# Optimization experiments

Measured on AMD Instinct MI355X. Metric: run time of the kernel, lower is better.

## Reference

```python
import jax, jax.numpy as jnp
import numpy as np

NUM_EMB = 512
LATENT = 128
TEXT_DIM = 512


def setup_inputs() -> dict:
    key = jax.random.key(0)
    ks = jax.random.split(key, 12)
    B, N = 64, 8192
    x = jax.random.normal(ks[0], (B, N, 3), dtype=jnp.float32)
    s = jax.random.normal(ks[1], (B, N), dtype=jnp.float32)
    e = jax.random.normal(ks[2], (B, TEXT_DIM), dtype=jnp.float32)
    # point_mlp: Linear(4,64) -> ReLU -> Linear(64,128); weights stored (in,out)
    W1 = jax.random.normal(ks[3], (4, 64), dtype=jnp.float32) * 0.5
    b1 = jnp.zeros((64,), dtype=jnp.float32)
    W2 = jax.random.normal(ks[4], (64, 128), dtype=jnp.float32) * 0.125
    b2 = jnp.zeros((128,), dtype=jnp.float32)
    # latent_mlp: Linear(128+512,256) -> ReLU -> Linear(256,128)
    W3 = jax.random.normal(ks[5], (128 + TEXT_DIM, 256), dtype=jnp.float32) * 0.04
    b3 = jnp.zeros((256,), dtype=jnp.float32)
    W4 = jax.random.normal(ks[6], (256, LATENT), dtype=jnp.float32) * 0.0625
    b4 = jnp.zeros((LATENT,), dtype=jnp.float32)
    # codebook init uniform(-1/K, 1/K) as in torch code
    codebook = jax.random.uniform(ks[7], (NUM_EMB, LATENT), dtype=jnp.float32,
                                  minval=-1.0 / NUM_EMB, maxval=1.0 / NUM_EMB)
    return {"x": x, "s": s, "e": e, "W1": W1, "b1": b1, "W2": W2, "b2": b2,
            "W3": W3, "b3": b3, "W4": W4, "b4": b4, "codebook": codebook}


def reference(x, s, e, W1, b1, W2, b2, W3, b3, W4, b4, codebook):
    # PointNet feature extraction
    point_inp = jnp.concatenate([x, s[..., None]], axis=-1)        # (B,N,4)
    h = jax.nn.relu(point_inp @ W1 + b1)                           # (B,N,64)
    point_feat = h @ W2 + b2                                       # (B,N,128)
    global_feat = jnp.max(point_feat, axis=1)                      # (B,128)
    combined = jnp.concatenate([global_feat, e], axis=-1)          # (B,640)
    z_e = jax.nn.relu(combined @ W3 + b3) @ W4 + b4                # (B,latent)
    # VQ: squared-L2 distances to codebook, argmin, gather
    dists = (jnp.sum(z_e * z_e, axis=1, keepdims=True)
             - 2.0 * (z_e @ codebook.T)
             + jnp.sum(codebook * codebook, axis=1))               # (B,K)
    indices = jnp.argmin(dists, axis=1)                            # (B,)
    z_q = codebook[indices]                                        # (B,latent)
    sg = jax.lax.stop_gradient
    codebook_loss = jnp.mean((z_q - sg(z_e)) ** 2)
    commitment_loss = jnp.mean((z_e - sg(z_q)) ** 2)
    z_q_st = z_e + sg(z_q - z_e)
    return (z_q_st, z_e, codebook_loss, commitment_loss, indices)
```

## Files before the change

### kernel.cpp

```cpp
#include <hip/hip_runtime.h>
#include <hip/hip_bf16.h>

typedef unsigned int u32;
typedef __attribute__((ext_vector_type(4))) unsigned int u32x4;
typedef __attribute__((ext_vector_type(8))) short s16x8;
typedef __attribute__((ext_vector_type(4))) float f32x4;

__device__ __forceinline__ u32 rne_hi(float a) {
    u32 u = __float_as_uint(a);
    return (u + 0x7FFFu + ((u >> 16) & 1u)) & 0xFFFF0000u;
}
__device__ __forceinline__ u32 pk_bf16(float a0, float a1) {
    __hip_bfloat162 pk2 = __float22bfloat162_rn(make_float2(a0, a1));
    u32 r;
    __builtin_memcpy(&r, &pk2, 4);
    return r;
}

__global__ __launch_bounds__(256, 4) void k1_pointfeat(
    const float* __restrict__ x, const float* __restrict__ s,
    const float* __restrict__ W1, const float* __restrict__ b1,
    const float* __restrict__ W2, float* __restrict__ ws_part)
{
    __shared__ __align__(16) u32 Hlds[2 * 2 * 64 * 32];
    const int tid   = threadIdx.x;
    const int lane  = tid & 63;
    const int point = tid & 63;
    const int kq    = __builtin_amdgcn_readfirstlane(tid >> 6);
    const int rl    = lane & 15;
    const int kg2   = lane >> 4;

    const int p0 = blockIdx.x * 512;

    s16x8 wbh[2][2], wbl[2][2];
    #pragma unroll
    for (int n = 0; n < 2; ++n)
        #pragma unroll
        for (int sl2 = 0; sl2 < 2; ++sl2)
            #pragma unroll
            for (int j = 0; j < 8; ++j) {
                float f = W2[(size_t)(kg2 * 8 + j + sl2 * 32) * 128 + kq * 32 + n * 16 + rl];
                u32 hb = rne_hi(f);
                float lo = f - __uint_as_float(hb);
                u32 lb = rne_hi(lo);
                wbh[n][sl2][j] = (short)(hb >> 16);
                wbl[n][sl2][j] = (short)(lb >> 16);
            }

    float rmax0 = -3.402823466e38f, rmax1 = -3.402823466e38f;

    const int wr0 = point * 32 + ((2 * kq)     ^ (point & 7)) * 4;
    const int wr1 = point * 32 + ((2 * kq + 1) ^ (point & 7)) * 4;

#define STAGE_COMPUTE(PX, PY, PZ, PW, VH0, VH1, VL0, VL1)                      \
    {                                                                          \
        _Pragma("unroll")                                                      \
        for (int h = 0; h < 2; ++h) {                                          \
            u32 hp[4], lp[4];                                                  \
            _Pragma("unroll")                                                  \
            for (int c = 0; c < 4; ++c) {                                      \
                const int k0 = kq * 16 + h * 8 + c * 2;                        \
                float a0 = fmaf(PX, W1[k0],                                    \
                           fmaf(PY, W1[64 + k0],                               \
                           fmaf(PZ, W1[128 + k0],                              \
                           fmaf(PW, W1[192 + k0], b1[k0]))));                  \
                float a1 = fmaf(PX, W1[k0 + 1],                                \
                           fmaf(PY, W1[65 + k0],                               \
                           fmaf(PZ, W1[129 + k0],                              \
                           fmaf(PW, W1[193 + k0], b1[k0 + 1]))));              \
                a0 = a0 > 0.f ? a0 : 0.f;                                      \
                a1 = a1 > 0.f ? a1 : 0.f;                                      \
                u32 ph = pk_bf16(a0, a1);                                      \
                float h0 = __uint_as_float(ph << 16);                          \
                float h1 = __uint_as_float(ph & 0xFFFF0000u);                  \
                u32 pl = pk_bf16(a0 - h0, a1 - h1);                            \
                hp[c] = ph; lp[c] = pl;                                        \
            }                                                                  \
            if (h == 0) { VH0 = (u32x4){hp[0],hp[1],hp[2],hp[3]};              \
                          VL0 = (u32x4){lp[0],lp[1],lp[2],lp[3]}; }            \
            else        { VH1 = (u32x4){hp[0],hp[1],hp[2],hp[3]};              \
                          VL1 = (u32x4){lp[0],lp[1],lp[2],lp[3]}; }            \
        }                                                                      \
    }
#define STAGE_WRITE(GG, VH0, VH1, VL0, VL1)                                    \
    {                                                                          \
        u32* Hw = &Hlds[((GG) & 1) * 4096];                                    \
        *(u32x4*)(Hw + wr0)        = VH0;                                      \
        *(u32x4*)(Hw + wr1)        = VH1;                                      \
        *(u32x4*)(Hw + 2048 + wr0) = VL0;                                      \
        *(u32x4*)(Hw + 2048 + wr1) = VL1;                                      \
    }

    {
        const int gp = p0 + point;
        float px = x[(size_t)gp * 3 + 0], py = x[(size_t)gp * 3 + 1];
        float pz = x[(size_t)gp * 3 + 2], pw = s[gp];
        u32x4 vh0, vh1, vl0, vl1;
        STAGE_COMPUTE(px, py, pz, pw, vh0, vh1, vl0, vl1)
        STAGE_WRITE(0, vh0, vh1, vl0, vl1)
    }
    float pxn, pyn, pzn, pwn;
    {
        const int gp = p0 + 64 + point;
        pxn = x[(size_t)gp * 3 + 0]; pyn = x[(size_t)gp * 3 + 1];
        pzn = x[(size_t)gp * 3 + 2]; pwn = s[gp];
    }

#define ARD(M, SL2) ((M) * 16 + rl) * 32 + ((((SL2) * 4 + kg2) ^ (rl & 7)) * 4)

    #pragma unroll 1
    for (int g = 0; g < 8; ++g) {
        __syncthreads();
        const u32* Hb = &Hlds[(g & 1) * 4096];

        s16x8 ah0[4], al0[4];
        #pragma unroll
        for (int m = 0; m < 4; ++m) {
            ah0[m] = *(const s16x8*)(Hb + ARD(m, 0));
            al0[m] = *(const s16x8*)(Hb + 2048 + ARD(m, 0));
        }

        u32x4 vh0, vh1, vl0, vl1;
        if (g < 7) {
            STAGE_COMPUTE(pxn, pyn, pzn, pwn, vh0, vh1, vl0, vl1)
        }

        f32x4 acc[4][2] = {};
        #pragma unroll
        for (int m = 0; m < 4; ++m)
            #pragma unroll
            for (int n = 0; n < 2; ++n)
                acc[m][n] = __builtin_amdgcn_mfma_f32_16x16x32_bf16(
                    ah0[m], wbh[n][0], acc[m][n], 0, 0, 0);
        #pragma unroll
        for (int m = 0; m < 4; ++m)
            #pragma unroll
            for (int n = 0; n < 2; ++n)
                acc[m][n] = __builtin_amdgcn_mfma_f32_16x16x32_bf16(
                    ah0[m], wbl[n][0], acc[m][n], 0, 0, 0);
        #pragma unroll
        for (int m = 0; m < 4; ++m)
            #pragma unroll
            for (int n = 0; n < 2; ++n)
                acc[m][n] = __builtin_amdgcn_mfma_f32_16x16x32_bf16(
                    al0[m], wbh[n][0], acc[m][n], 0, 0, 0);

        s16x8 ah1[4], al1[4];
        #pragma unroll
        for (int m = 0; m < 4; ++m) {
            ah1[m] = *(const s16x8*)(Hb + ARD(m, 1));
            al1[m] = *(const s16x8*)(Hb + 2048 + ARD(m, 1));
        }
        if (g < 6) {
            const int gp = p0 + (g + 2) * 64 + point;
            pxn = x[(size_t)gp * 3 + 0]; pyn = x[(size_t)gp * 3 + 1];
            pzn = x[(size_t)gp * 3 + 2]; pwn = s[gp];
        }

        #pragma unroll
        for (int m = 0; m < 4; ++m)
            #pragma unroll
            for (int n = 0; n < 2; ++n)
                acc[m][n] = __builtin_amdgcn_mfma_f32_16x16x32_bf16(
                    ah1[m], wbh[n][1], acc[m][n], 0, 0, 0);
        #pragma unroll
        for (int m = 0; m < 4; ++m)
            #pragma unroll
            for (int n = 0; n < 2; ++n)
                acc[m][n] = __builtin_amdgcn_mfma_f32_16x16x32_bf16(
                    ah1[m], wbl[n][1], acc[m][n], 0, 0, 0);
        #pragma unroll
        for (int m = 0; m < 4; ++m)
            #pragma unroll
            for (int n = 0; n < 2; ++n)
                acc[m][n] = __builtin_amdgcn_mfma_f32_16x16x32_bf16(
                    al1[m], wbh[n][1], acc[m][n], 0, 0, 0);

        if (g < 7) {
            STAGE_WRITE(g + 1, vh0, vh1, vl0, vl1)
        }

        #pragma unroll
        for (int m = 0; m < 4; ++m)
            #pragma unroll
            for (int r = 0; r < 4; ++r) {
                rmax0 = fmaxf(rmax0, acc[m][0][r]);
                rmax1 = fmaxf(rmax1, acc[m][1][r]);
            }
    }
#undef ARD
#undef STAGE_COMPUTE
#undef STAGE_WRITE

    rmax0 = fmaxf(rmax0, __shfl_xor(rmax0, 16, 64));
    rmax0 = fmaxf(rmax0, __shfl_xor(rmax0, 32, 64));
    rmax1 = fmaxf(rmax1, __shfl_xor(rmax1, 16, 64));
    rmax1 = fmaxf(rmax1, __shfl_xor(rmax1, 32, 64));
    if (lane < 16) {
        ws_part[blockIdx.x * 128 + kq * 32 + lane]      = rmax0;
        ws_part[blockIdx.x * 128 + kq * 32 + 16 + lane] = rmax1;
    }
}

__global__ __launch_bounds__(256) void k2a_hidden(
    const float* __restrict__ ws_part, const float* __restrict__ b2,
    const float* __restrict__ e,
    const float* __restrict__ W3, const float* __restrict__ b3,
    float* __restrict__ ws_hid)
{
    const int blk = blockIdx.x;
    const int b   = blk >> 2;
    const int c   = blk & 3;
    const int tid = threadIdx.x;
    const int u   = tid & 63;
    const int part = tid >> 6;
    __shared__ float comb[640];
    __shared__ float psum[4][64];

    for (int i = tid; i < 640; i += 256) {
        float v;
        if (i < 128) {
            const float* __restrict__ pp = ws_part + (size_t)b * 16 * 128 + i;
            float m = pp[0];
            #pragma unroll
            for (int t = 1; t < 16; ++t) m = fmaxf(m, pp[t * 128]);
            v = m + b2[i];
        } else {
            v = e[b * 512 + (i - 128)];
        }
        comb[i] = v;
    }
    __syncthreads();

    const int gu = c * 64 + u;
    const float* __restrict__ Wp = W3 + (size_t)(part * 160) * 256 + gu;
    const float* __restrict__ cp = comb + part * 160;
    float a = 0.f;
    for (int i = 0; i < 160; ++i) a = fmaf(cp[i], Wp[(size_t)i * 256], a);
    psum[part][u] = a;
    __syncthreads();
    if (tid < 64) {
        float hv = psum[0][u] + psum[1][u] + psum[2][u] + psum[3][u] + b3[gu];
        ws_hid[b * 256 + gu] = hv > 0.f ? hv : 0.f;
    }
}

__global__ __launch_bounds__(512) void k2b_vq(
    const float* __restrict__ ws_hid,
    const float* __restrict__ W4, const float* __restrict__ b4,
    const float* __restrict__ cb, float* __restrict__ out,
    float* __restrict__ ws_loss)
{
    const int b = blockIdx.x, tid = threadIdx.x;
    __shared__ float hid[256];
    __shared__ float psum[4][128];
    __shared__ float ze[128];
    __shared__ float red_d[512];
    __shared__ int   red_i[512];
    __shared__ float lred[128];
    __shared__ float zzs;

    if (tid < 256) hid[tid] = ws_hid[b * 256 + tid];
    __syncthreads();

    {
        const int u = tid & 127, part = tid >> 7;
        const float* __restrict__ Wp = W4 + (size_t)(part * 64) * 128 + u;
        const float* __restrict__ hp = hid + part * 64;
        float a = 0.f;
        for (int i = 0; i < 64; ++i) a = fmaf(hp[i], Wp[(size_t)i * 128], a);
        psum[part][u] = a;
    }
    __syncthreads();
    if (tid < 128) {
        float a = psum[0][tid] + psum[1][tid] + psum[2][tid] + psum[3][tid] + b4[tid];
        ze[tid] = a;
        out[8192 + b * 128 + tid] = a;
    }
    __syncthreads();

    if (tid < 64) {
        float t = ze[tid] * ze[tid] + ze[tid + 64] * ze[tid + 64];
        #pragma unroll
        for (int d = 1; d < 64; d <<= 1) t += __shfl_xor(t, d, 64);
        if (tid == 0) zzs = t;
    }
    __syncthreads();

    {
        float dot = 0.f, cc = 0.f;
        const f32x4* __restrict__ cp = (const f32x4*)(cb + (size_t)tid * 128);
        for (int k4 = 0; k4 < 32; ++k4) {
            f32x4 v = cp[k4];
            dot = fmaf(ze[k4 * 4 + 0], v.x, dot);
            cc  = fmaf(v.x, v.x, cc);
            dot = fmaf(ze[k4 * 4 + 1], v.y, dot);
            cc  = fmaf(v.y, v.y, cc);
            dot = fmaf(ze[k4 * 4 + 2], v.z, dot);
            cc  = fmaf(v.z, v.z, cc);
            dot = fmaf(ze[k4 * 4 + 3], v.w, dot);
            cc  = fmaf(v.w, v.w, cc);
        }
        red_d[tid] = zzs - 2.f * dot + cc;
        red_i[tid] = tid;
    }
    __syncthreads();

    for (int sft = 256; sft >= 1; sft >>= 1) {
        if (tid < sft) {
            float da = red_d[tid], db = red_d[tid + sft];
            int   ia = red_i[tid], ib = red_i[tid + sft];
            if (db < da || (db == da && ib < ia)) { red_d[tid] = db; red_i[tid] = ib; }
        }
        __syncthreads();
    }
    const int bc = red_i[0];

    if (tid < 128) {
        float zq  = cb[(size_t)bc * 128 + tid];
        float zev = ze[tid];
        out[b * 128 + tid] = zev + (zq - zev);
        float d = zq - zev;
        lred[tid] = d * d;
    }
    if (tid == 0) out[16386 + b] = (float)bc;
    __syncthreads();
    if (tid < 64) {
        float t = lred[tid] + lred[tid + 64];
        #pragma unroll
        for (int d = 1; d < 64; d <<= 1) t += __shfl_xor(t, d, 64);
        if (tid == 0) ws_loss[b] = t;
    }
}

__global__ void k3_loss(const float* __restrict__ ws_loss, float* __restrict__ out)
{
    const int t = threadIdx.x;
    float v = ws_loss[t];
    #pragma unroll
    for (int d = 1; d < 64; d <<= 1) v += __shfl_xor(v, d, 64);
    if (t == 0) {
        float m = v / 8192.f;
        out[16384] = m;
        out[16385] = m;
    }
}

extern "C" void kernel_launch(void* const* d_in, const int* in_sizes, int n_in,
                              void* d_out, int out_size, void* d_ws, size_t ws_size,
                              hipStream_t stream) {
    const float* x  = (const float*)d_in[0];
    const float* s  = (const float*)d_in[1];
    const float* e  = (const float*)d_in[2];
    const float* W1 = (const float*)d_in[3];
    const float* b1 = (const float*)d_in[4];
    const float* W2 = (const float*)d_in[5];
    const float* b2 = (const float*)d_in[6];
    const float* W3 = (const float*)d_in[7];
    const float* b3 = (const float*)d_in[8];
    const float* W4 = (const float*)d_in[9];
    const float* b4 = (const float*)d_in[10];
    const float* cb = (const float*)d_in[11];
    float* out = (float*)d_out;

    float* ws_part = (float*)d_ws;
    float* ws_hid  = (float*)d_ws + 1024 * 128;
    float* ws_loss = (float*)d_ws + 1024 * 128 + 64 * 256;

    k1_pointfeat<<<1024, 256, 0, stream>>>(x, s, W1, b1, W2, ws_part);
    k2a_hidden<<<256, 256, 0, stream>>>(ws_part, b2, e, W3, b3, ws_hid);
    k2b_vq<<<64, 512, 0, stream>>>(ws_hid, W4, b4, cb, out, ws_loss);
    k3_loss<<<1, 64, 0, stream>>>(ws_loss, out);
}
```

Before: 47.60 us.

## Retile point-MLP MFMA per wave and fuse hidden and VQ head kernels

Each wave in the point-feature kernel now covers a 32-point by 64-channel tile instead of 64 points by 32 channels. That halves the LDS fragment reads per wave but doubles the per-wave W2 register fragments, so occupancy is lowered to 3 blocks per SIMD. Partial maxima are written per M-half, which doubles the partial buffer and the reduction count. The separate latent-MLP hidden kernel and VQ kernel are fused into one 1024-thread block per batch item, removing a launch and the hidden-state round trip through global memory, at the cost of fewer blocks doing the W3 product.

```diff
diff --git a/kernel.cpp b/kernel.cpp
--- a/kernel.cpp
+++ b/kernel.cpp
@@ -17,7 +17,7 @@
     return r;
 }
 
-__global__ __launch_bounds__(256, 4) void k1_pointfeat(
+__global__ __launch_bounds__(256, 3) void k1_pointfeat(
     const float* __restrict__ x, const float* __restrict__ s,
     const float* __restrict__ W1, const float* __restrict__ b1,
     const float* __restrict__ W2, float* __restrict__ ws_part)
@@ -27,19 +27,21 @@
     const int lane  = tid & 63;
     const int point = tid & 63;
     const int kq    = __builtin_amdgcn_readfirstlane(tid >> 6);
+    const int mh    = kq >> 1;
+    const int nh    = kq & 1;
     const int rl    = lane & 15;
     const int kg2   = lane >> 4;
 
     const int p0 = blockIdx.x * 512;
 
-    s16x8 wbh[2][2], wbl[2][2];
+    s16x8 wbh[4][2], wbl[4][2];
     #pragma unroll
-    for (int n = 0; n < 2; ++n)
+    for (int n = 0; n < 4; ++n)
         #pragma unroll
         for (int sl2 = 0; sl2 < 2; ++sl2)
             #pragma unroll
             for (int j = 0; j < 8; ++j) {
-                float f = W2[(size_t)(kg2 * 8 + j + sl2 * 32) * 128 + kq * 32 + n * 16 + rl];
+                float f = W2[(size_t)(kg2 * 8 + j + sl2 * 32) * 128 + nh * 64 + n * 16 + rl];
                 u32 hb = rne_hi(f);
                 float lo = f - __uint_as_float(hb);
                 u32 lb = rne_hi(lo);
@@ -47,7 +49,8 @@
                 wbl[n][sl2][j] = (short)(lb >> 16);
             }
 
-    float rmax0 = -3.402823466e38f, rmax1 = -3.402823466e38f;
+    float rmaxn[4] = {-3.402823466e38f, -3.402823466e38f,
+                      -3.402823466e38f, -3.402823466e38f};
 
     const int wr0 = point * 32 + ((2 * kq)     ^ (point & 7)) * 4;
     const int wr1 = point * 32 + ((2 * kq + 1) ^ (point & 7)) * 4;
@@ -108,16 +111,18 @@
 
 #define ARD(M, SL2) ((M) * 16 + rl) * 32 + ((((SL2) * 4 + kg2) ^ (rl & 7)) * 4)
 
+    const int mh2 = mh * 2;
+
     #pragma unroll 1
     for (int g = 0; g < 8; ++g) {
         __syncthreads();
         const u32* Hb = &Hlds[(g & 1) * 4096];
 
-        s16x8 ah0[4], al0[4];
-        #pragma unroll
-        for (int m = 0; m < 4; ++m) {
-            ah0[m] = *(const s16x8*)(Hb + ARD(m, 0));
-            al0[m] = *(const s16x8*)(Hb + 2048 + ARD(m, 0));
+        s16x8 ah0[2], al0[2];
+        #pragma unroll
+        for (int m = 0; m < 2; ++m) {
+            ah0[m] = *(const s16x8*)(Hb + ARD(mh2 + m, 0));
+            al0[m] = *(const s16x8*)(Hb + 2048 + ARD(mh2 + m, 0));
         }
 
         u32x4 vh0, vh1, vl0, vl1;
@@ -125,31 +130,31 @@
             STAGE_COMPUTE(pxn, pyn, pzn, pwn, vh0, vh1, vl0, vl1)
         }
 
-        f32x4 acc[4][2] = {};
-        #pragma unroll
-        for (int m = 0; m < 4; ++m)
-            #pragma unroll
-            for (int n = 0; n < 2; ++n)
+        f32x4 acc[2][4] = {};
+        #pragma unroll
+        for (int m = 0; m < 2; ++m)
+            #pragma unroll
+            for (int n = 0; n < 4; ++n)
                 acc[m][n] = __builtin_amdgcn_mfma_f32_16x16x32_bf16(
                     ah0[m], wbh[n][0], acc[m][n], 0, 0, 0);
         #pragma unroll
-        for (int m = 0; m < 4; ++m)
-            #pragma unroll
-            for (int n = 0; n < 2; ++n)
+        for (int m = 0; m < 2; ++m)
+            #pragma unroll
+            for (int n = 0; n < 4; ++n)
                 acc[m][n] = __builtin_amdgcn_mfma_f32_16x16x32_bf16(
                     ah0[m], wbl[n][0], acc[m][n], 0, 0, 0);
         #pragma unroll
-        for (int m = 0; m < 4; ++m)
-            #pragma unroll
-            for (int n = 0; n < 2; ++n)
+        for (int m = 0; m < 2; ++m)
+            #pragma unroll
+            for (int n = 0; n < 4; ++n)
                 acc[m][n] = __builtin_amdgcn_mfma_f32_16x16x32_bf16(
                     al0[m], wbh[n][0], acc[m][n], 0, 0, 0);
 
-        s16x8 ah1[4], al1[4];
-        #pragma unroll
-        for (int m = 0; m < 4; ++m) {
-            ah1[m] = *(const s16x8*)(Hb + ARD(m, 1));
-            al1[m] = *(const s16x8*)(Hb + 2048 + ARD(m, 1));
+        s16x8 ah1[2], al1[2];
+        #pragma unroll
+        for (int m = 0; m < 2; ++m) {
+            ah1[m] = *(const s16x8*)(Hb + ARD(mh2 + m, 1));
+            al1[m] = *(const s16x8*)(Hb + 2048 + ARD(mh2 + m, 1));
         }
         if (g < 6) {
             const int gp = p0 + (g + 2) * 64 + point;
@@ -158,21 +163,21 @@
         }
 
         #pragma unroll
-        for (int m = 0; m < 4; ++m)
-            #pragma unroll
-            for (int n = 0; n < 2; ++n)
+        for (int m = 0; m < 2; ++m)
+            #pragma unroll
+            for (int n = 0; n < 4; ++n)
                 acc[m][n] = __builtin_amdgcn_mfma_f32_16x16x32_bf16(
                     ah1[m], wbh[n][1], acc[m][n], 0, 0, 0);
         #pragma unroll
-        for (int m = 0; m < 4; ++m)
-            #pragma unroll
-            for (int n = 0; n < 2; ++n)
+        for (int m = 0; m < 2; ++m)
+            #pragma unroll
+            for (int n = 0; n < 4; ++n)
                 acc[m][n] = __builtin_amdgcn_mfma_f32_16x16x32_bf16(
                     ah1[m], wbl[n][1], acc[m][n], 0, 0, 0);
         #pragma unroll
-        for (int m = 0; m < 4; ++m)
-            #pragma unroll
-            for (int n = 0; n < 2; ++n)
+        for (int m = 0; m < 2; ++m)
+            #pragma unroll
+            for (int n = 0; n < 4; ++n)
                 acc[m][n] = __builtin_amdgcn_mfma_f32_16x16x32_bf16(
                     al1[m], wbh[n][1], acc[m][n], 0, 0, 0);
 
@@ -181,89 +186,78 @@
         }
 
         #pragma unroll
-        for (int m = 0; m < 4; ++m)
-            #pragma unroll
-            for (int r = 0; r < 4; ++r) {
-                rmax0 = fmaxf(rmax0, acc[m][0][r]);
-                rmax1 = fmaxf(rmax1, acc[m][1][r]);
-            }
+        for (int m = 0; m < 2; ++m)
+            #pragma unroll
+            for (int n = 0; n < 4; ++n)
+                #pragma unroll
+                for (int r = 0; r < 4; ++r)
+                    rmaxn[n] = fmaxf(rmaxn[n], acc[m][n][r]);
     }
 #undef ARD
 #undef STAGE_COMPUTE
 #undef STAGE_WRITE
 
-    rmax0 = fmaxf(rmax0, __shfl_xor(rmax0, 16, 64));
-    rmax0 = fmaxf(rmax0, __shfl_xor(rmax0, 32, 64));
-    rmax1 = fmaxf(rmax1, __shfl_xor(rmax1, 16, 64));
-    rmax1 = fmaxf(rmax1, __shfl_xor(rmax1, 32, 64));
+    #pragma unroll
+    for (int n = 0; n < 4; ++n) {
+        rmaxn[n] = fmaxf(rmaxn[n], __shfl_xor(rmaxn[n], 16, 64));
+        rmaxn[n] = fmaxf(rmaxn[n], __shfl_xor(rmaxn[n], 32, 64));
+    }
     if (lane < 16) {
-        ws_part[blockIdx.x * 128 + kq * 32 + lane]      = rmax0;
-        ws_part[blockIdx.x * 128 + kq * 32 + 16 + lane] = rmax1;
-    }
-}
-
-__global__ __launch_bounds__(256) void k2a_hidden(
+        #pragma unroll
+        for (int n = 0; n < 4; ++n)
+            ws_part[blockIdx.x * 256 + mh * 128 + nh * 64 + n * 16 + lane] = rmaxn[n];
+    }
+}
+
+__global__ __launch_bounds__(1024) void k2_head(
     const float* __restrict__ ws_part, const float* __restrict__ b2,
     const float* __restrict__ e,
     const float* __restrict__ W3, const float* __restrict__ b3,
-    float* __restrict__ ws_hid)
-{
-    const int blk = blockIdx.x;
-    const int b   = blk >> 2;
-    const int c   = blk & 3;
-    const int tid = threadIdx.x;
-    const int u   = tid & 63;
-    const int part = tid >> 6;
-    __shared__ float comb[640];
-    __shared__ float psum[4][64];
-
-    for (int i = tid; i < 640; i += 256) {
-        float v;
-        if (i < 128) {
-            const float* __restrict__ pp = ws_part + (size_t)b * 16 * 128 + i;
-            float m = pp[0];
-            #pragma unroll
-            for (int t = 1; t < 16; ++t) m = fmaxf(m, pp[t * 128]);
-            v = m + b2[i];
-        } else {
-            v = e[b * 512 + (i - 128)];
-        }
-        comb[i] = v;
-    }
-    __syncthreads();
-
-    const int gu = c * 64 + u;
-    const float* __restrict__ Wp = W3 + (size_t)(part * 160) * 256 + gu;
-    const float* __restrict__ cp = comb + part * 160;
-    float a = 0.f;
-    for (int i = 0; i < 160; ++i) a = fmaf(cp[i], Wp[(size_t)i * 256], a);
-    psum[part][u] = a;
-    __syncthreads();
-    if (tid < 64) {
-        float hv = psum[0][u] + psum[1][u] + psum[2][u] + psum[3][u] + b3[gu];
-        ws_hid[b * 256 + gu] = hv > 0.f ? hv : 0.f;
-    }
-}
-
-__global__ __launch_bounds__(512) void k2b_vq(
-    const float* __restrict__ ws_hid,
     const float* __restrict__ W4, const float* __restrict__ b4,
     const float* __restrict__ cb, float* __restrict__ out,
     float* __restrict__ ws_loss)
 {
     const int b = blockIdx.x, tid = threadIdx.x;
+    __shared__ float comb[640];
+    __shared__ float psum[4][256];
     __shared__ float hid[256];
-    __shared__ float psum[4][128];
     __shared__ float ze[128];
     __shared__ float red_d[512];
     __shared__ int   red_i[512];
     __shared__ float lred[128];
     __shared__ float zzs;
 
-    if (tid < 256) hid[tid] = ws_hid[b * 256 + tid];
+    if (tid < 640) {
+        float v;
+        if (tid < 128) {
+            const float* __restrict__ pp = ws_part + (size_t)b * 4096 + tid;
+            float m = pp[0];
+            #pragma unroll
+            for (int t = 1; t < 32; ++t) m = fmaxf(m, pp[t * 128]);
+            v = m + b2[tid];
+        } else {
+            v = e[b * 512 + (tid - 128)];
+        }
+        comb[tid] = v;
+    }
     __syncthreads();
 
     {
+        const int u = tid & 255, part = tid >> 8;
+        const float* __restrict__ Wp = W3 + (size_t)(part * 160) * 256 + u;
+        const float* __restrict__ cp = comb + part * 160;
+        float a = 0.f;
+        for (int i = 0; i < 160; ++i) a = fmaf(cp[i], Wp[(size_t)i * 256], a);
+        psum[part][u] = a;
+    }
+    __syncthreads();
+    if (tid < 256) {
+        float hv = psum[0][tid] + psum[1][tid] + psum[2][tid] + psum[3][tid] + b3[tid];
+        hid[tid] = hv > 0.f ? hv : 0.f;
+    }
+    __syncthreads();
+
+    if (tid < 512) {
         const int u = tid & 127, part = tid >> 7;
         const float* __restrict__ Wp = W4 + (size_t)(part * 64) * 128 + u;
         const float* __restrict__ hp = hid + part * 64;
@@ -287,7 +281,7 @@
     }
     __syncthreads();
 
-    {
+    if (tid < 512) {
         float dot = 0.f, cc = 0.f;
         const f32x4* __restrict__ cp = (const f32x4*)(cb + (size_t)tid * 128);
         for (int k4 = 0; k4 < 32; ++k4) {
@@ -364,11 +358,9 @@
     float* out = (float*)d_out;
 
     float* ws_part = (float*)d_ws;
-    float* ws_hid  = (float*)d_ws + 1024 * 128;
-    float* ws_loss = (float*)d_ws + 1024 * 128 + 64 * 256;
+    float* ws_loss = (float*)d_ws + 1024 * 256;
 
     k1_pointfeat<<<1024, 256, 0, stream>>>(x, s, W1, b1, W2, ws_part);
-    k2a_hidden<<<256, 256, 0, stream>>>(ws_part, b2, e, W3, b3, ws_hid);
-    k2b_vq<<<64, 512, 0, stream>>>(ws_hid, W4, b4, cb, out, ws_loss);
+    k2_head<<<64, 1024, 0, stream>>>(ws_part, b2, e, W3, b3, W4, b4, cb, out, ws_loss);
     k3_loss<<<1, 64, 0, stream>>>(ws_loss, out);
 }
```

Result: slower. 50.66 us (+6.4%).

## Fuse hidden-layer and VQ head kernels into one 1024-thread block per batch

Applied to the files above, without the earlier changes.

Merges the W3 hidden-layer kernel and the W4/VQ kernel into a single kernel with one 1024-thread block per batch row. The hidden activations now stay in shared memory instead of going through a workspace buffer, and one kernel launch and its inter-kernel gap disappear. In exchange, the W3 matvec runs on 64 blocks instead of 256, so each block reads all of W3 and parallelism in that stage drops. Threads 512 and above sit idle during the VQ phase.

```diff
diff --git a/kernel.cpp b/kernel.cpp
--- a/kernel.cpp
+++ b/kernel.cpp
@@ -202,68 +202,55 @@
     }
 }
 
-__global__ __launch_bounds__(256) void k2a_hidden(
+__global__ __launch_bounds__(1024) void k2_head(
     const float* __restrict__ ws_part, const float* __restrict__ b2,
     const float* __restrict__ e,
     const float* __restrict__ W3, const float* __restrict__ b3,
-    float* __restrict__ ws_hid)
-{
-    const int blk = blockIdx.x;
-    const int b   = blk >> 2;
-    const int c   = blk & 3;
-    const int tid = threadIdx.x;
-    const int u   = tid & 63;
-    const int part = tid >> 6;
-    __shared__ float comb[640];
-    __shared__ float psum[4][64];
-
-    for (int i = tid; i < 640; i += 256) {
-        float v;
-        if (i < 128) {
-            const float* __restrict__ pp = ws_part + (size_t)b * 16 * 128 + i;
-            float m = pp[0];
-            #pragma unroll
-            for (int t = 1; t < 16; ++t) m = fmaxf(m, pp[t * 128]);
-            v = m + b2[i];
-        } else {
-            v = e[b * 512 + (i - 128)];
-        }
-        comb[i] = v;
-    }
-    __syncthreads();
-
-    const int gu = c * 64 + u;
-    const float* __restrict__ Wp = W3 + (size_t)(part * 160) * 256 + gu;
-    const float* __restrict__ cp = comb + part * 160;
-    float a = 0.f;
-    for (int i = 0; i < 160; ++i) a = fmaf(cp[i], Wp[(size_t)i * 256], a);
-    psum[part][u] = a;
-    __syncthreads();
-    if (tid < 64) {
-        float hv = psum[0][u] + psum[1][u] + psum[2][u] + psum[3][u] + b3[gu];
-        ws_hid[b * 256 + gu] = hv > 0.f ? hv : 0.f;
-    }
-}
-
-__global__ __launch_bounds__(512) void k2b_vq(
-    const float* __restrict__ ws_hid,
     const float* __restrict__ W4, const float* __restrict__ b4,
     const float* __restrict__ cb, float* __restrict__ out,
     float* __restrict__ ws_loss)
 {
     const int b = blockIdx.x, tid = threadIdx.x;
+    __shared__ float comb[640];
+    __shared__ float psum[4][256];
     __shared__ float hid[256];
-    __shared__ float psum[4][128];
     __shared__ float ze[128];
     __shared__ float red_d[512];
     __shared__ int   red_i[512];
     __shared__ float lred[128];
     __shared__ float zzs;
 
-    if (tid < 256) hid[tid] = ws_hid[b * 256 + tid];
+    if (tid < 640) {
+        float v;
+        if (tid < 128) {
+            const float* __restrict__ pp = ws_part + (size_t)b * 16 * 128 + tid;
+            float m = pp[0];
+            #pragma unroll
+            for (int t = 1; t < 16; ++t) m = fmaxf(m, pp[t * 128]);
+            v = m + b2[tid];
+        } else {
+            v = e[b * 512 + (tid - 128)];
+        }
+        comb[tid] = v;
+    }
     __syncthreads();
 
     {
+        const int u = tid & 255, part = tid >> 8;
+        const float* __restrict__ Wp = W3 + (size_t)(part * 160) * 256 + u;
+        const float* __restrict__ cp = comb + part * 160;
+        float a = 0.f;
+        for (int i = 0; i < 160; ++i) a = fmaf(cp[i], Wp[(size_t)i * 256], a);
+        psum[part][u] = a;
+    }
+    __syncthreads();
+    if (tid < 256) {
+        float hv = psum[0][tid] + psum[1][tid] + psum[2][tid] + psum[3][tid] + b3[tid];
+        hid[tid] = hv > 0.f ? hv : 0.f;
+    }
+    __syncthreads();
+
+    if (tid < 512) {
         const int u = tid & 127, part = tid >> 7;
         const float* __restrict__ Wp = W4 + (size_t)(part * 64) * 128 + u;
         const float* __restrict__ hp = hid + part * 64;
@@ -287,7 +274,7 @@
     }
     __syncthreads();
 
-    {
+    if (tid < 512) {
         float dot = 0.f, cc = 0.f;
         const f32x4* __restrict__ cp = (const f32x4*)(cb + (size_t)tid * 128);
         for (int k4 = 0; k4 < 32; ++k4) {
@@ -364,11 +351,9 @@
     float* out = (float*)d_out;
 
     float* ws_part = (float*)d_ws;
-    float* ws_hid  = (float*)d_ws + 1024 * 128;
-    float* ws_loss = (float*)d_ws + 1024 * 128 + 64 * 256;
+    float* ws_loss = (float*)d_ws + 1024 * 128;
 
     k1_pointfeat<<<1024, 256, 0, stream>>>(x, s, W1, b1, W2, ws_part);
-    k2a_hidden<<<256, 256, 0, stream>>>(ws_part, b2, e, W3, b3, ws_hid);
-    k2b_vq<<<64, 512, 0, stream>>>(ws_hid, W4, b4, cb, out, ws_loss);
+    k2_head<<<64, 1024, 0, stream>>>(ws_part, b2, e, W3, b3, W4, b4, cb, out, ws_loss);
     k3_loss<<<1, 64, 0, stream>>>(ws_loss, out);
 }
```

After: 47.98 us. About the same (+0.8%).
